# Optimization experiments

Hardware: AMD Instinct MI355X
Metric: run time of the kernel (lower is better)

## Reference

```python
import jax, jax.numpy as jnp
import numpy as np

INF = 1e10  # stands in for +inf in fp32-safe squared-distance field


def _dt1d_sq(f):
    """Exact 1D squared Euclidean distance transform along the last axis.
    f: (..., N) squared-distance field (0 on seeds, INF elsewhere).
    D[..., i] = min_j (i-j)^2 + f[..., j]  (brute-force lower envelope, exact).
    Uses lax.map over output index i to avoid an (..., N, N) intermediate.
    """
    N = f.shape[-1]
    idx = jnp.arange(N)

    def body(i):
        return jnp.min(f + ((i - idx) ** 2).astype(f.dtype), axis=-1)

    out = jax.lax.map(body, idx)  # (N, ...)
    return jnp.moveaxis(out, 0, -1)


def _edt(mask):
    """scipy.ndimage.distance_transform_edt(1 - mask) per (b, c):
    Euclidean distance to nearest mask==1 pixel; all-zeros if channel empty.
    mask: (B, C, H, W) binary float.
    """
    f = jnp.where(mask > 0.5, 0.0, INF)
    d = _dt1d_sq(f)                              # sweep along W
    d = _dt1d_sq(jnp.swapaxes(d, -1, -2))        # sweep along H
    d = jnp.sqrt(jnp.swapaxes(d, -1, -2))
    empty = jnp.sum(mask, axis=(-1, -2), keepdims=True) == 0
    return jnp.where(empty, 0.0, d)


def _boundary(x):
    """|2D laplacian| per channel with zero padding=1. x: (B, C, H, W)."""
    xp = jnp.pad(x, ((0, 0), (0, 0), (1, 1), (1, 1)))
    lap = (xp[:, :, :-2, 1:-1] + xp[:, :, 2:, 1:-1]
           + xp[:, :, 1:-1, :-2] + xp[:, :, 1:-1, 2:] - 4.0 * x)
    return jnp.abs(lap)


def setup_inputs() -> dict:
    key = jax.random.key(0)
    k1, k2 = jax.random.split(key)
    B, C, H, W = 8, 4, 256, 256
    pred = jax.random.normal(k1, (B, C, H, W), dtype=jnp.float32)
    target = jax.random.randint(k2, (B, H, W), 0, C, dtype=jnp.int64)
    return {"pred": pred, "target": target}


def reference(pred, target):
    C = pred.shape[1]
    p = jax.nn.softmax(pred, axis=1)                       # (B,C,H,W)
    t1h = jax.nn.one_hot(target, C, axis=1, dtype=p.dtype) # (B,C,H,W)
    target_dist = _edt(t1h)
    pred_boundary = _boundary(p)
    loss = jnp.sum(pred_boundary * target_dist) / jnp.sum(pred_boundary)
    return loss
```

## Files before the change

kernel.cpp:

```cpp
#include <hip/hip_runtime.h>

#define NB 8
#define NC 4
#define NH 256
#define NW 256
#define HW (NH * NW)
#define CHW (NC * HW)
#define INFV 1e10f
#define TH 4
#define MAIN_BLOCKS (NB * (NH / TH))
#define WR (TH + 8)

__global__ __launch_bounds__(256) void k_edt_w(const int* __restrict__ tgt,
                                               unsigned short* __restrict__ D16) {
    int bh = blockIdx.x;
    int i  = threadIdx.x;
    int wv = i >> 6;
    int ln = i & 63;

    int tv = tgt[(size_t)bh * NW + i];

    __shared__ unsigned long long mk[NC][4];
    #pragma unroll
    for (int c = 0; c < NC; ++c) {
        unsigned long long m = __ballot(tv == c);
        if (ln == 0) mk[c][wv] = m;
    }
    __syncthreads();

    unsigned long long le = (ln == 63) ? ~0ull : ((1ull << (ln + 1)) - 1ull);
    unsigned long long ge = ~0ull << ln;

    unsigned short res[NC];
    #pragma unroll
    for (int c = 0; c < NC; ++c) {
        int jl = -1000;
        #pragma unroll
        for (int k = 0; k < 4; ++k) {
            unsigned long long x = mk[c][k];
            x = (k > wv) ? 0ull : ((k == wv) ? (x & le) : x);
            if (x) jl = k * 64 + 63 - __clzll((long long)x);
        }
        int jr = 1000;
        #pragma unroll
        for (int k = 3; k >= 0; --k) {
            unsigned long long x = mk[c][k];
            x = (k < wv) ? 0ull : ((k == wv) ? (x & ge) : x);
            if (x) jr = k * 64 + __ffsll((unsigned long long)x) - 1;
        }
        int dl = i - jl;
        int dr = jr - i;
        int dd = min(dl, dr);
        res[c] = (dd > 255) ? (unsigned short)65535
                            : (unsigned short)(dd * dd);
    }

    int b = bh >> 8;
    int h = bh & 255;
    size_t o = (size_t)b * CHW + (size_t)h * NW + i;
    D16[o]          = res[0];
    D16[o + HW]     = res[1];
    D16[o + 2 * HW] = res[2];
    D16[o + 3 * HW] = res[3];
}

__device__ __forceinline__ void softmax4(const float* __restrict__ pred_b,
                                         int hw, float o[NC]) {
    float x0 = pred_b[hw];
    float x1 = pred_b[hw + HW];
    float x2 = pred_b[hw + 2 * HW];
    float x3 = pred_b[hw + 3 * HW];
    float m  = fmaxf(fmaxf(x0, x1), fmaxf(x2, x3));
    float e0 = __expf(x0 - m);
    float e1 = __expf(x1 - m);
    float e2 = __expf(x2 - m);
    float e3 = __expf(x3 - m);
    float inv = 1.0f / (e0 + e1 + e2 + e3);
    o[0] = e0 * inv; o[1] = e1 * inv; o[2] = e2 * inv; o[3] = e3 * inv;
}

__global__ __launch_bounds__(256) void k_main(const float* __restrict__ pred,
                                              const unsigned short* __restrict__ D16,
                                              float2* __restrict__ partial) {
    int blk  = blockIdx.x;
    int b    = blk >> 6;
    int tile = blk & 63;
    int h0   = tile * TH;
    int w    = threadIdx.x;

    const unsigned short* Db = D16 + (size_t)b * CHW + w;
    const float* pred_b = pred + (size_t)b * CHW;

    float win[WR][NC];
    #pragma unroll
    for (int k = 0; k < WR; ++k) {
        int j = h0 - 4 + k;
        bool ok = (unsigned)j < (unsigned)NH;
        #pragma unroll
        for (int c = 0; c < NC; ++c) {
            unsigned short u = ok ? Db[(size_t)c * HW + (j << 8)]
                                  : (unsigned short)65535;
            win[k][c] = (u > 65025) ? INFV : (float)u;
        }
    }

    __shared__ float ps[NC][TH + 2][NW + 2];
    for (int pos = threadIdx.x; pos < (TH + 2) * (NW + 2); pos += 256) {
        int row = pos / (NW + 2);
        int col = pos - row * (NW + 2);
        int gy  = h0 - 1 + row;
        int gx  = col - 1;
        float o[NC] = {0.0f, 0.0f, 0.0f, 0.0f};
        if ((unsigned)gy < (unsigned)NH && (unsigned)gx < (unsigned)NW)
            softmax4(pred_b, (gy << 8) + gx, o);
        ps[0][row][col] = o[0];
        ps[1][row][col] = o[1];
        ps[2][row][col] = o[2];
        ps[3][row][col] = o[3];
    }
    __syncthreads();

    float num = 0.0f, den = 0.0f;
    #pragma unroll
    for (int r = 0; r < TH; ++r) {
        int h = h0 + r;
        #pragma unroll
        for (int c = 0; c < NC; ++c) {
            float lap = fabsf(ps[c][r][w + 1] + ps[c][r + 2][w + 1]
                            + ps[c][r + 1][w] + ps[c][r + 1][w + 2]
                            - 4.0f * ps[c][r + 1][w + 1]);

            float best = win[r + 4][c];
            #pragma unroll
            for (int dr = 1; dr <= 4; ++dr) {
                float rr = (float)(dr * dr);
                best = fminf(best, rr + win[r + 4 - dr][c]);
                best = fminf(best, rr + win[r + 4 + dr][c]);
            }

            if (best > 25.0f) {
                const unsigned short* f = Db + (size_t)c * HW;
                for (int r2 = 5; r2 < NH; ++r2) {
                    float rr = (float)(r2 * r2);
                    if (rr >= best) break;
                    int hu = h - r2, hd = h + r2;
                    if (hu >= 0) {
                        unsigned short u = f[hu << 8];
                        if (u <= 65025) best = fminf(best, rr + (float)u);
                    }
                    if (hd < NH) {
                        unsigned short u = f[hd << 8];
                        if (u <= 65025) best = fminf(best, rr + (float)u);
                    }
                }
            }

            float dv = (best > 1e8f) ? 0.0f : sqrtf(best);
            num += lap * dv;
            den += lap;
        }
    }

    #pragma unroll
    for (int off = 32; off > 0; off >>= 1) {
        num += __shfl_down(num, off);
        den += __shfl_down(den, off);
    }
    __shared__ float sn[4], sd[4];
    int lane = threadIdx.x & 63;
    int wvi  = threadIdx.x >> 6;
    if (lane == 0) { sn[wvi] = num; sd[wvi] = den; }
    __syncthreads();
    if (threadIdx.x == 0) {
        partial[blockIdx.x] = make_float2(sn[0] + sn[1] + sn[2] + sn[3],
                                          sd[0] + sd[1] + sd[2] + sd[3]);
    }
}

__global__ __launch_bounds__(256) void k_final(const float2* __restrict__ partial,
                                               float* __restrict__ out) {
    double n = 0.0, d = 0.0;
    for (int i = threadIdx.x; i < MAIN_BLOCKS; i += 256) {
        float2 v = partial[i];
        n += (double)v.x;
        d += (double)v.y;
    }
    #pragma unroll
    for (int off = 32; off > 0; off >>= 1) {
        n += __shfl_down(n, off);
        d += __shfl_down(d, off);
    }
    __shared__ double snd[4], sdd[4];
    int lane = threadIdx.x & 63;
    int wv   = threadIdx.x >> 6;
    if (lane == 0) { snd[wv] = n; sdd[wv] = d; }
    __syncthreads();
    if (threadIdx.x == 0) {
        double nn = snd[0] + snd[1] + snd[2] + snd[3];
        double dd = sdd[0] + sdd[1] + sdd[2] + sdd[3];
        out[0] = (float)(nn / dd);
    }
}

extern "C" void kernel_launch(void* const* d_in, const int* in_sizes, int n_in,
                              void* d_out, int out_size, void* d_ws, size_t ws_size,
                              hipStream_t stream) {
    const float* pred = (const float*)d_in[0];
    const int*   tgt  = (const int*)d_in[1];
    float*       out  = (float*)d_out;

    unsigned short* D16     = (unsigned short*)d_ws;
    float2*         partial = (float2*)((char*)d_ws + (size_t)NB * CHW * 2);

    k_edt_w<<<NB * NH,     256, 0, stream>>>(tgt, D16);
    k_main <<<MAIN_BLOCKS, 256, 0, stream>>>(pred, D16, partial);
    k_final<<<1,           256, 0, stream>>>(partial, out);
}
```

Baseline: 24.78 us.

## Halve row tile, fully unroll branchless halo softmax, clamp window loads

Reduces rows per block from 4 to 2, doubling the block count so more blocks are resident across the CUs, and adds an occupancy hint to the launch bounds. The halo softmax loop becomes a fixed 5-iteration unrolled loop with clamped indices and a select instead of a branch, so loads can be issued together. Window loads use clamped row indices instead of conditional loads. Halving the tile increases redundant halo softmax and window loads per output row relative to useful work.

```diff
diff --git a/kernel.cpp b/kernel.cpp
--- a/kernel.cpp
+++ b/kernel.cpp
@@ -7,9 +7,10 @@
 #define HW (NH * NW)
 #define CHW (NC * HW)
 #define INFV 1e10f
-#define TH 4
+#define TH 2
 #define MAIN_BLOCKS (NB * (NH / TH))
 #define WR (TH + 8)
+#define HALO ((TH + 2) * (NW + 2))
 
 __global__ __launch_bounds__(256) void k_edt_w(const int* __restrict__ tgt,
                                                unsigned short* __restrict__ D16) {
@@ -48,9 +49,7 @@
             x = (k < wv) ? 0ull : ((k == wv) ? (x & ge) : x);
             if (x) jr = k * 64 + __ffsll((unsigned long long)x) - 1;
         }
-        int dl = i - jl;
-        int dr = jr - i;
-        int dd = min(dl, dr);
+        int dd = min(i - jl, jr - i);
         res[c] = (dd > 255) ? (unsigned short)65535
                             : (unsigned short)(dd * dd);
     }
@@ -79,12 +78,12 @@
     o[0] = e0 * inv; o[1] = e1 * inv; o[2] = e2 * inv; o[3] = e3 * inv;
 }
 
-__global__ __launch_bounds__(256) void k_main(const float* __restrict__ pred,
-                                              const unsigned short* __restrict__ D16,
-                                              float2* __restrict__ partial) {
+__global__ __launch_bounds__(256, 4) void k_main(const float* __restrict__ pred,
+                                                 const unsigned short* __restrict__ D16,
+                                                 float2* __restrict__ partial) {
     int blk  = blockIdx.x;
-    int b    = blk >> 6;
-    int tile = blk & 63;
+    int b    = blk >> 7;
+    int tile = blk & 127;
     int h0   = tile * TH;
     int w    = threadIdx.x;
 
@@ -94,29 +93,36 @@
     float win[WR][NC];
     #pragma unroll
     for (int k = 0; k < WR; ++k) {
-        int j = h0 - 4 + k;
+        int j   = h0 - 4 + k;
         bool ok = (unsigned)j < (unsigned)NH;
+        int jc  = min(max(j, 0), NH - 1);
         #pragma unroll
         for (int c = 0; c < NC; ++c) {
-            unsigned short u = ok ? Db[(size_t)c * HW + (j << 8)]
-                                  : (unsigned short)65535;
-            win[k][c] = (u > 65025) ? INFV : (float)u;
+            unsigned short u = Db[(size_t)c * HW + (jc << 8)];
+            win[k][c] = (!ok || u > 65025) ? INFV : (float)u;
         }
     }
 
     __shared__ float ps[NC][TH + 2][NW + 2];
-    for (int pos = threadIdx.x; pos < (TH + 2) * (NW + 2); pos += 256) {
-        int row = pos / (NW + 2);
-        int col = pos - row * (NW + 2);
+    #pragma unroll
+    for (int k = 0; k < 5; ++k) {
+        int pos   = threadIdx.x + k * 256;
+        int pos_c = min(pos, HALO - 1);
+        int row = pos_c / (NW + 2);
+        int col = pos_c - row * (NW + 2);
         int gy  = h0 - 1 + row;
         int gx  = col - 1;
-        float o[NC] = {0.0f, 0.0f, 0.0f, 0.0f};
-        if ((unsigned)gy < (unsigned)NH && (unsigned)gx < (unsigned)NW)
-            softmax4(pred_b, (gy << 8) + gx, o);
-        ps[0][row][col] = o[0];
-        ps[1][row][col] = o[1];
-        ps[2][row][col] = o[2];
-        ps[3][row][col] = o[3];
+        bool valid = (unsigned)gy < (unsigned)NH && (unsigned)gx < (unsigned)NW;
+        int gyc = min(max(gy, 0), NH - 1);
+        int gxc = min(max(gx, 0), NW - 1);
+        float o[NC];
+        softmax4(pred_b, (gyc << 8) + gxc, o);
+        if (pos < HALO) {
+            ps[0][row][col] = valid ? o[0] : 0.0f;
+            ps[1][row][col] = valid ? o[1] : 0.0f;
+            ps[2][row][col] = valid ? o[2] : 0.0f;
+            ps[3][row][col] = valid ? o[3] : 0.0f;
+        }
     }
     __syncthreads();
 
```

Measured after the change: 27.34 us. +10.3%, slower.

## Interleave per-channel distance field and fuse final reduction via last-block atomic

Applied to the files above, without the earlier changes.

The 1D distance field is now stored channel-interleaved, so each pixel's four 16-bit values are written and read as a single 8-byte access instead of four strided loads. The final reduction kernel is removed: each main block increments an atomic counter and the last block to finish sums the partials. This saves one kernel launch but adds a memset launch, and the far-search loads in the slow path become strided by four channels.

```diff
diff --git a/kernel.cpp b/kernel.cpp
--- a/kernel.cpp
+++ b/kernel.cpp
@@ -12,7 +12,7 @@
 #define WR (TH + 8)
 
 __global__ __launch_bounds__(256) void k_edt_w(const int* __restrict__ tgt,
-                                               unsigned short* __restrict__ D16) {
+                                               unsigned short* __restrict__ Dp) {
     int bh = blockIdx.x;
     int i  = threadIdx.x;
     int wv = i >> 6;
@@ -31,7 +31,7 @@
     unsigned long long le = (ln == 63) ? ~0ull : ((1ull << (ln + 1)) - 1ull);
     unsigned long long ge = ~0ull << ln;
 
-    unsigned short res[NC];
+    unsigned res[NC];
     #pragma unroll
     for (int c = 0; c < NC; ++c) {
         int jl = -1000;
@@ -48,20 +48,14 @@
             x = (k < wv) ? 0ull : ((k == wv) ? (x & ge) : x);
             if (x) jr = k * 64 + __ffsll((unsigned long long)x) - 1;
         }
-        int dl = i - jl;
-        int dr = jr - i;
-        int dd = min(dl, dr);
-        res[c] = (dd > 255) ? (unsigned short)65535
-                            : (unsigned short)(dd * dd);
-    }
-
-    int b = bh >> 8;
-    int h = bh & 255;
-    size_t o = (size_t)b * CHW + (size_t)h * NW + i;
-    D16[o]          = res[0];
-    D16[o + HW]     = res[1];
-    D16[o + 2 * HW] = res[2];
-    D16[o + 3 * HW] = res[3];
+        int dd = min(i - jl, jr - i);
+        res[c] = (dd > 255) ? 65535u : (unsigned)(dd * dd);
+    }
+
+    uint2 pk;
+    pk.x = res[0] | (res[1] << 16);
+    pk.y = res[2] | (res[3] << 16);
+    *(uint2*)(Dp + ((size_t)bh * NW + i) * NC) = pk;
 }
 
 __device__ __forceinline__ void softmax4(const float* __restrict__ pred_b,
@@ -80,28 +74,32 @@
 }
 
 __global__ __launch_bounds__(256) void k_main(const float* __restrict__ pred,
-                                              const unsigned short* __restrict__ D16,
-                                              float2* __restrict__ partial) {
+                                              const unsigned short* __restrict__ Dp,
+                                              float2* __restrict__ partial,
+                                              unsigned* __restrict__ cnt,
+                                              float* __restrict__ out) {
     int blk  = blockIdx.x;
     int b    = blk >> 6;
     int tile = blk & 63;
     int h0   = tile * TH;
     int w    = threadIdx.x;
 
-    const unsigned short* Db = D16 + (size_t)b * CHW + w;
     const float* pred_b = pred + (size_t)b * CHW;
 
     float win[WR][NC];
     #pragma unroll
     for (int k = 0; k < WR; ++k) {
-        int j = h0 - 4 + k;
+        int j   = h0 - 4 + k;
         bool ok = (unsigned)j < (unsigned)NH;
-        #pragma unroll
-        for (int c = 0; c < NC; ++c) {
-            unsigned short u = ok ? Db[(size_t)c * HW + (j << 8)]
-                                  : (unsigned short)65535;
-            win[k][c] = (u > 65025) ? INFV : (float)u;
-        }
+        uint2 v;
+        if (ok) v = *(const uint2*)(Dp + (((size_t)b * NH + j) * NW + w) * NC);
+        else    { v.x = 0xFFFFFFFFu; v.y = 0xFFFFFFFFu; }
+        unsigned a0 = v.x & 0xFFFFu, a1 = v.x >> 16;
+        unsigned a2 = v.y & 0xFFFFu, a3 = v.y >> 16;
+        win[k][0] = (a0 > 65025u) ? INFV : (float)a0;
+        win[k][1] = (a1 > 65025u) ? INFV : (float)a1;
+        win[k][2] = (a2 > 65025u) ? INFV : (float)a2;
+        win[k][3] = (a3 > 65025u) ? INFV : (float)a3;
     }
 
     __shared__ float ps[NC][TH + 2][NW + 2];
@@ -139,17 +137,18 @@
             }
 
             if (best > 25.0f) {
-                const unsigned short* f = Db + (size_t)c * HW;
+                const unsigned short* f = Dp + (size_t)b * NH * NW * NC
+                                        + (size_t)w * NC + c;
                 for (int r2 = 5; r2 < NH; ++r2) {
                     float rr = (float)(r2 * r2);
                     if (rr >= best) break;
                     int hu = h - r2, hd = h + r2;
                     if (hu >= 0) {
-                        unsigned short u = f[hu << 8];
+                        unsigned short u = f[(size_t)hu * NW * NC];
                         if (u <= 65025) best = fminf(best, rr + (float)u);
                     }
                     if (hd < NH) {
-                        unsigned short u = f[hd << 8];
+                        unsigned short u = f[(size_t)hd * NW * NC];
                         if (u <= 65025) best = fminf(best, rr + (float)u);
                     }
                 }
@@ -171,34 +170,38 @@
     int wvi  = threadIdx.x >> 6;
     if (lane == 0) { sn[wvi] = num; sd[wvi] = den; }
     __syncthreads();
+
+    __shared__ bool amLast;
     if (threadIdx.x == 0) {
         partial[blockIdx.x] = make_float2(sn[0] + sn[1] + sn[2] + sn[3],
                                           sd[0] + sd[1] + sd[2] + sd[3]);
-    }
-}
-
-__global__ __launch_bounds__(256) void k_final(const float2* __restrict__ partial,
-                                               float* __restrict__ out) {
-    double n = 0.0, d = 0.0;
-    for (int i = threadIdx.x; i < MAIN_BLOCKS; i += 256) {
-        float2 v = partial[i];
-        n += (double)v.x;
-        d += (double)v.y;
-    }
-    #pragma unroll
-    for (int off = 32; off > 0; off >>= 1) {
-        n += __shfl_down(n, off);
-        d += __shfl_down(d, off);
-    }
-    __shared__ double snd[4], sdd[4];
-    int lane = threadIdx.x & 63;
-    int wv   = threadIdx.x >> 6;
-    if (lane == 0) { snd[wv] = n; sdd[wv] = d; }
-    __syncthreads();
-    if (threadIdx.x == 0) {
-        double nn = snd[0] + snd[1] + snd[2] + snd[3];
-        double dd = sdd[0] + sdd[1] + sdd[2] + sdd[3];
-        out[0] = (float)(nn / dd);
+        __threadfence();
+        unsigned old = atomicAdd(cnt, 1u);
+        amLast = (old == MAIN_BLOCKS - 1);
+    }
+    __syncthreads();
+
+    if (amLast) {
+        __threadfence();
+        double n = 0.0, d = 0.0;
+        for (int i = threadIdx.x; i < MAIN_BLOCKS; i += 256) {
+            float2 v = partial[i];
+            n += (double)v.x;
+            d += (double)v.y;
+        }
+        #pragma unroll
+        for (int off = 32; off > 0; off >>= 1) {
+            n += __shfl_down(n, off);
+            d += __shfl_down(d, off);
+        }
+        __shared__ double snd[4], sdd[4];
+        if (lane == 0) { snd[wvi] = n; sdd[wvi] = d; }
+        __syncthreads();
+        if (threadIdx.x == 0) {
+            double nn = snd[0] + snd[1] + snd[2] + snd[3];
+            double dd = sdd[0] + sdd[1] + sdd[2] + sdd[3];
+            out[0] = (float)(nn / dd);
+        }
     }
 }
 
@@ -209,10 +212,11 @@
     const int*   tgt  = (const int*)d_in[1];
     float*       out  = (float*)d_out;
 
-    unsigned short* D16     = (unsigned short*)d_ws;
+    unsigned short* Dp      = (unsigned short*)d_ws;
     float2*         partial = (float2*)((char*)d_ws + (size_t)NB * CHW * 2);
-
-    k_edt_w<<<NB * NH,     256, 0, stream>>>(tgt, D16);
-    k_main <<<MAIN_BLOCKS, 256, 0, stream>>>(pred, D16, partial);
-    k_final<<<1,           256, 0, stream>>>(partial, out);
-}
+    unsigned*       cnt     = (unsigned*)(partial + MAIN_BLOCKS);
+
+    hipMemsetAsync(cnt, 0, sizeof(unsigned), stream);
+    k_edt_w<<<NB * NH,     256, 0, stream>>>(tgt, Dp);
+    k_main <<<MAIN_BLOCKS, 256, 0, stream>>>(pred, Dp, partial, cnt, out);
+}
```

Result: slower. 37.71 us (+52.2%).
